# Kernel optimization log

Hardware: AMD Instinct MI355X
Metric: run time of the kernel (lower is better)

The kernel has to match this reference:

```python
import jax, jax.numpy as jnp
import numpy as np

HIDDEN = 4096
NH = 32          # num attention heads
NKV = 8          # num key/value heads
HD = HIDDEN // NH  # 128
THETA = 10000.0
WINDOW = 4096    # sliding window hard-coded in forward


def _rotate_half(x):
    x1, x2 = jnp.split(x, 2, axis=-1)
    return jnp.concatenate((-x2, x1), axis=-1)


def setup_inputs() -> dict:
    key = jax.random.key(0)
    ks = jax.random.split(key, 5)
    B, S = 1, 2048
    hidden_states = jax.random.normal(ks[0], (B, S, HIDDEN), jnp.float32)
    position_ids = jnp.broadcast_to(jnp.arange(S, dtype=jnp.int64), (B, S))
    s = 0.02
    q_w = jax.random.normal(ks[1], (HIDDEN, NH * HD), jnp.float32) * s
    k_w = jax.random.normal(ks[2], (HIDDEN, NKV * HD), jnp.float32) * s
    v_w = jax.random.normal(ks[3], (HIDDEN, NKV * HD), jnp.float32) * s
    o_w = jax.random.normal(ks[4], (NH * HD, HIDDEN), jnp.float32) * s
    return {"hidden_states": hidden_states, "position_ids": position_ids,
            "q_w": q_w, "k_w": k_w, "v_w": v_w, "o_w": o_w}


def reference(hidden_states, position_ids, q_w, k_w, v_w, o_w):
    B, S, _ = hidden_states.shape
    # projections (bias=False), split heads -> [B, H, S, D]
    q = (hidden_states @ q_w).reshape(B, S, NH, HD).transpose(0, 2, 1, 3)
    k = (hidden_states @ k_w).reshape(B, S, NKV, HD).transpose(0, 2, 1, 3)
    v = (hidden_states @ v_w).reshape(B, S, NKV, HD).transpose(0, 2, 1, 3)

    # rotary embedding cache (MistralRotaryEmbedding)
    inv_freq = 1.0 / (THETA ** (jnp.arange(0, HD, 2, dtype=jnp.float32) / HD))
    t = jnp.arange(S, dtype=jnp.float32)
    freqs = t[:, None] * inv_freq[None, :]           # [S, HD/2]
    emb = jnp.concatenate((freqs, freqs), axis=-1)   # [S, HD]
    cos = jnp.cos(emb)[position_ids][:, None]        # [B, 1, S, HD]
    sin = jnp.sin(emb)[position_ids][:, None]
    q = q * cos + _rotate_half(q) * sin
    k = k * cos + _rotate_half(k) * sin

    # GQA repeat_kv: [B, NKV, S, D] -> [B, NH, S, D]
    rep = NH // NKV
    k = jnp.repeat(k, rep, axis=1)
    v = jnp.repeat(v, rep, axis=1)

    # scores + sliding-window causal mask
    scale = 1.0 / np.sqrt(HD).astype(np.float32)
    w = jnp.einsum("bhqd,bhkd->bhqk", q, k) * scale  # [B, NH, S, S]
    i = jnp.arange(S)[:, None]
    j = jnp.arange(S)[None, :]
    allowed = (j <= i) & ((i - j) < WINDOW)
    neg = jnp.finfo(jnp.float32).min
    w = w + jnp.where(allowed, 0.0, neg)[None, None]

    # fp32 softmax (upcast as in HF Mistral)
    w = jax.nn.softmax(w.astype(jnp.float32), axis=-1).astype(q.dtype)

    out = jnp.einsum("bhqk,bhkd->bhqd", w, v)        # [B, NH, S, D]
    out = out.transpose(0, 2, 1, 3).reshape(B, S, NH * HD)
    return out @ o_w                                  # [B, S, HIDDEN]
```

## Files before the change

kernel.cpp:

```cpp
#include <hip/hip_runtime.h>
#include <hip/hip_bf16.h>

#define S 2048
#define HID 4096
#define NH 32
#define NKV 8
#define HD 128
#define QKVN 6144

typedef __attribute__((ext_vector_type(8))) short bf16x8;
typedef __attribute__((ext_vector_type(4))) float f32x4;
typedef __attribute__((ext_vector_type(8))) unsigned short u16x8;
typedef __attribute__((ext_vector_type(4))) unsigned short u16x4;

#define GLOAD16(src, dst)                                                        \
  __builtin_amdgcn_global_load_lds(                                              \
      (const __attribute__((address_space(1))) unsigned int*)(src),              \
      (__attribute__((address_space(3))) unsigned int*)(dst), 16, 0, 0)

__device__ __forceinline__ unsigned short f2bf(float f) {
  union { float f; unsigned u; } c; c.f = f;
  unsigned u = c.u;
  return (unsigned short)((u + 0x7FFFu + ((u >> 16) & 1u)) >> 16);
}
__device__ __forceinline__ float bf2f(unsigned short h) {
  union { unsigned u; float f; } c; c.u = ((unsigned)h) << 16;
  return c.f;
}

__global__ void convert_kernel(const float* __restrict__ in,
                               unsigned short* __restrict__ out, int n4) {
  int i = blockIdx.x * blockDim.x + threadIdx.x;
  if (i < n4) {
    float4 v = ((const float4*)in)[i];
    ushort4 o;
    o.x = f2bf(v.x); o.y = f2bf(v.y); o.z = f2bf(v.z); o.w = f2bf(v.w);
    ((ushort4*)out)[i] = o;
  }
}

__global__ void transpose_convert(const float* __restrict__ in,
                                  unsigned short* __restrict__ out, int N) {
  __shared__ float tile[32][33];
  int tx = threadIdx.x, ty = threadIdx.y;
  int n0 = blockIdx.x * 32, k0 = blockIdx.y * 32;
#pragma unroll
  for (int i = 0; i < 32; i += 8)
    tile[ty + i][tx] = in[(size_t)(k0 + ty + i) * N + n0 + tx];
  __syncthreads();
#pragma unroll
  for (int i = 0; i < 32; i += 8)
    out[(size_t)(n0 + ty + i) * HID + k0 + tx] = f2bf(tile[tx][ty + i]);
}

__device__ __forceinline__ void storeC(unsigned short* C, size_t idx, float v) { C[idx] = f2bf(v); }
__device__ __forceinline__ void storeC(float* C, size_t idx, float v) { C[idx] = v; }

template <typename OutT>
__launch_bounds__(256, 2)
__global__ void gemm_bt(const unsigned short* __restrict__ A,
                        const unsigned short* __restrict__ Bt,
                        OutT* __restrict__ C, int K, int ldc) {
  __shared__ unsigned short As[2][2][128 * 32];
  __shared__ unsigned short Bs[2][2][128 * 32];
  const int tid = threadIdx.x, lane = tid & 63, w = tid >> 6;
  const int wr = w >> 1, wc = w & 1;
  const int m0 = blockIdx.y * 128, n0 = blockIdx.x * 128;
  const int lq = lane & 15, g = lane >> 4;
  const int swz8 = (g ^ (lq & 3) ^ ((lq >> 2) & 3)) << 3;

  f32x4 acc[4][4] = {};
  const int NT = K >> 6;

  auto STAGE_PAIR = [&](int bb, int ss, int kt) {
#pragma unroll
    for (int i = 0; i < 2; ++i) {
      int ci = tid + i * 256;
      int row = ci >> 2;
      int jl = (((ci & 3) ^ (row & 3) ^ ((row >> 2) & 3))) << 3;
      GLOAD16(A + (size_t)(m0 + row) * K + kt + ss * 32 + jl, &As[bb][ss][ci * 8]);
      GLOAD16(Bt + (size_t)(n0 + row) * K + kt + ss * 32 + jl, &Bs[bb][ss][ci * 8]);
    }
  };

  STAGE_PAIR(0, 0, 0);
  STAGE_PAIR(0, 1, 0);

  for (int t = 0; t < NT; ++t) {
    const int c = t & 1;
    const bool more = (t + 1) < NT;
    const int kt1 = (t + 1) << 6;
#pragma unroll
    for (int s = 0; s < 2; ++s) {
      if (s == 0 || more) asm volatile("s_waitcnt vmcnt(4)" ::: "memory");
      else                asm volatile("s_waitcnt vmcnt(0)" ::: "memory");
      __builtin_amdgcn_s_barrier();

      bf16x8 af[4], bfr[4];
#pragma unroll
      for (int mi = 0; mi < 4; ++mi)
        af[mi] = *(const bf16x8*)&As[c][s][(wr * 64 + mi * 16 + lq) * 32 + swz8];
#pragma unroll
      for (int ni = 0; ni < 4; ++ni)
        bfr[ni] = *(const bf16x8*)&Bs[c][s][(wc * 64 + ni * 16 + lq) * 32 + swz8];

      if (more) STAGE_PAIR(c ^ 1, s, kt1);

      asm volatile("s_waitcnt lgkmcnt(0)" ::: "memory");
      __builtin_amdgcn_sched_barrier(0);
      __builtin_amdgcn_s_setprio(1);
#pragma unroll
      for (int mi = 0; mi < 4; ++mi)
#pragma unroll
        for (int ni = 0; ni < 4; ++ni)
          acc[mi][ni] = __builtin_amdgcn_mfma_f32_16x16x32_bf16(af[mi], bfr[ni], acc[mi][ni], 0, 0, 0);
      __builtin_amdgcn_s_setprio(0);
    }
  }

#pragma unroll
  for (int mi = 0; mi < 4; ++mi) {
#pragma unroll
    for (int ni = 0; ni < 4; ++ni) {
      int row = m0 + wr * 64 + mi * 16 + g * 4;
      int col = n0 + wc * 64 + ni * 16 + lq;
#pragma unroll
      for (int r = 0; r < 4; ++r)
        storeC(C, (size_t)(row + r) * ldc + col, acc[mi][ni][r]);
    }
  }
}

__global__ void rope_kernel(unsigned short* __restrict__ qkv) {
  int idx = blockIdx.x * blockDim.x + threadIdx.x;
  int d = idx & 63;
  int h = (idx >> 6) % (NH + NKV);
  int s = (idx >> 6) / (NH + NKV);
  size_t base = (size_t)s * QKVN + (h < NH ? h * HD : NH * HD + (h - NH) * HD);
  float invf = __expf(-(float)d * (1.0f / 64.0f) * 9.210340371976184f);
  float ang = (float)s * invf;
  float c, sn;
  __sincosf(ang, &sn, &c);
  float x1 = bf2f(qkv[base + d]);
  float x2 = bf2f(qkv[base + d + 64]);
  float o1 = x1 * c - x2 * sn;
  float o2 = x2 * c + x1 * sn;
  if (h < NH) {
    o1 *= 0.08838834764831845f;
    o2 *= 0.08838834764831845f;
  }
  qkv[base + d] = f2bf(o1);
  qkv[base + d + 64] = f2bf(o2);
}

__launch_bounds__(512, 4)
__global__ void attn_kernel(const unsigned short* __restrict__ qkv,
                            unsigned short* __restrict__ ao) {
  __shared__ unsigned short Ks[2][64 * 128];
  __shared__ unsigned short Vt[128 * 88];
  __shared__ unsigned short Ps[8][16 * 88];

  const int tid = threadIdx.x, lane = tid & 63, w = tid >> 6;
  const int b = blockIdx.x;
  const int h = blockIdx.y;
  const int qblk = (h < 16) ? (15 - b) : b;
  const int kh = h >> 2;
  const int lq = lane & 15, g = lane >> 4;
  const int qbase = qblk * 128 + w * 16;
  const size_t koff = (size_t)NH * HD + (size_t)kh * HD;
  const size_t voff = (size_t)(NH + NKV) * HD + (size_t)kh * HD;

  bf16x8 qf[4];
  {
    const unsigned short* qp = qkv + (size_t)(qbase + lq) * QKVN + (size_t)h * HD + g * 8;
#pragma unroll
    for (int ks = 0; ks < 4; ++ks) qf[ks] = *(const bf16x8*)(qp + ks * 32);
  }

  f32x4 o[8] = {};
  float m = -1e30f;
  float l = 0.f;

  auto KSTAGE = [&](int bb, int kv0) {
#pragma unroll
    for (int i = 0; i < 2; ++i) {
      int kvk = (w * 2 + i) * 4 + (lane >> 4);
      int chl = (lane & 15) ^ (kvk & 7);
      GLOAD16(qkv + (size_t)(kv0 + kvk) * QKVN + koff + chl * 8, &Ks[bb][(w * 2 + i) * 512]);
    }
  };
  const int vd0 = (tid & 31) * 4;
  const int vkv = (tid >> 5) * 4;
  u16x4 vr[4];
  auto VLOAD = [&](int kv0) {
#pragma unroll
    for (int i = 0; i < 4; ++i)
      vr[i] = *(const u16x4*)(qkv + (size_t)(kv0 + vkv + i) * QKVN + voff + vd0);
  };
  auto VWRITE = [&]() {
#pragma unroll
    for (int j = 0; j < 4; ++j) {
      const int d = vd0 + j;
      const int vswz = ((d >> 3) & 3) << 1;
      const int vcol = (((vkv >> 2) ^ vswz) << 2);
      u16x4 val = {vr[0][j], vr[1][j], vr[2][j], vr[3][j]};
      *(u16x4*)&Vt[d * 88 + vcol] = val;
    }
  };

  unsigned short* Pw = &Ps[w][0];
  const int nt = qblk * 2 + 2;

  KSTAGE(0, 0);
  VLOAD(0);
  int cur = 0;
  for (int t = 0; t < nt; ++t) {
    const int kv0 = t * 64;
    __syncthreads();
    VWRITE();
    __syncthreads();
    if (t + 1 < nt) { KSTAGE(cur ^ 1, kv0 + 64); VLOAD(kv0 + 64); }

    const int nraw = qbase + 16 - kv0;
    const int nact = nraw > 64 ? 64 : nraw;

    f32x4 sc[4];
    __builtin_amdgcn_s_setprio(1);
#pragma unroll
    for (int st = 0; st < 4; ++st) {
      if (st * 16 < nact) {
        f32x4 s = {};
#pragma unroll
        for (int ks = 0; ks < 4; ++ks) {
          const bf16x8 kf = *(const bf16x8*)
              &Ks[cur][(st * 16 + lq) * 128 + (((ks * 4 + g) ^ (lq & 7)) << 3)];
          s = __builtin_amdgcn_mfma_f32_16x16x32_bf16(kf, qf[ks], s, 0, 0, 0);
        }
        sc[st] = s;
      } else {
        sc[st] = (f32x4){-1e30f, -1e30f, -1e30f, -1e30f};
      }
    }
    __builtin_amdgcn_s_setprio(0);
    if (nraw < 79) {
      const int q = qbase + lq;
#pragma unroll
      for (int st = 0; st < 4; ++st) {
        int kv = kv0 + st * 16 + g * 4;
#pragma unroll
        for (int r = 0; r < 4; ++r)
          if (kv + r > q) sc[st][r] = -1e30f;
      }
    }

    float mn = fmaxf(fmaxf(fmaxf(sc[0][0], sc[0][1]), fmaxf(sc[0][2], sc[0][3])),
                     fmaxf(fmaxf(sc[1][0], sc[1][1]), fmaxf(sc[1][2], sc[1][3])));
    mn = fmaxf(mn, fmaxf(fmaxf(fmaxf(sc[2][0], sc[2][1]), fmaxf(sc[2][2], sc[2][3])),
                         fmaxf(fmaxf(sc[3][0], sc[3][1]), fmaxf(sc[3][2], sc[3][3]))));
    mn = fmaxf(mn, __shfl_xor(mn, 16, 64));
    mn = fmaxf(mn, __shfl_xor(mn, 32, 64));
    const bool need = __any(mn > m);
    const float m2 = fmaxf(m, mn);
    const float alpha = __expf(m - m2);
    m = m2;
    float rs = 0.f;
#pragma unroll
    for (int st = 0; st < 4; ++st)
#pragma unroll
      for (int r = 0; r < 4; ++r) {
        float p = __expf(sc[st][r] - m2);
        sc[st][r] = p;
        rs += p;
      }
    rs += __shfl_xor(rs, 16, 64);
    rs += __shfl_xor(rs, 32, 64);
    l = l * alpha + rs;

    if (need) {
      float alphaR[4];
#pragma unroll
      for (int r = 0; r < 4; ++r) alphaR[r] = __shfl(alpha, g * 4 + r, 64);
#pragma unroll
      for (int p = 0; p < 8; ++p)
#pragma unroll
        for (int r = 0; r < 4; ++r) o[p][r] *= alphaR[r];
    }

#pragma unroll
    for (int st = 0; st < 4; ++st) {
      u16x4 val = {f2bf(sc[st][0]), f2bf(sc[st][1]), f2bf(sc[st][2]), f2bf(sc[st][3])};
      *(u16x4*)&Pw[lq * 88 + st * 16 + g * 4] = val;
    }

    const int nks = nact > 0 ? (nact + 31) >> 5 : 0;
    __builtin_amdgcn_s_setprio(1);
    for (int ks = 0; ks < nks; ++ks) {
      const bf16x8 pf = *(const bf16x8*)&Pw[lq * 88 + ks * 32 + g * 8];
#pragma unroll
      for (int p = 0; p < 8; ++p) {
        const int d = p * 16 + lq;
        const int rswz = ((d >> 3) & 3) << 1;
        const int kvc = (ks * 8 + g * 2) ^ rswz;
        const bf16x8 vf = *(const bf16x8*)&Vt[d * 88 + (kvc << 2)];
        o[p] = __builtin_amdgcn_mfma_f32_16x16x32_bf16(pf, vf, o[p], 0, 0, 0);
      }
    }
    __builtin_amdgcn_s_setprio(0);

    cur ^= 1;
  }

  float invR[4];
#pragma unroll
  for (int r = 0; r < 4; ++r) invR[r] = 1.0f / __shfl(l, g * 4 + r, 64);
#pragma unroll
  for (int p = 0; p < 8; ++p)
#pragma unroll
    for (int r = 0; r < 4; ++r)
      ao[(size_t)(qbase + g * 4 + r) * (NH * HD) + (size_t)h * HD + p * 16 + lq] =
          f2bf(o[p][r] * invR[r]);
}

extern "C" void kernel_launch(void* const* d_in, const int* in_sizes, int n_in,
                              void* d_out, int out_size, void* d_ws, size_t ws_size,
                              hipStream_t stream) {
  const float* X  = (const float*)d_in[0];
  const float* qw = (const float*)d_in[2];
  const float* kw = (const float*)d_in[3];
  const float* vw = (const float*)d_in[4];
  const float* ow = (const float*)d_in[5];
  float* out = (float*)d_out;

  char* ws = (char*)d_ws;
  unsigned short* Xb  = (unsigned short*)(ws);
  unsigned short* Wt  = (unsigned short*)(ws + (size_t)(16u << 20));
  unsigned short* QKV = (unsigned short*)(ws + (size_t)(64u << 20));
  unsigned short* AO  = (unsigned short*)(ws + (size_t)(88u << 20));
  unsigned short* OWt = (unsigned short*)(ws);

  dim3 tb(32, 8);

  convert_kernel<<<(S * HID / 4 + 255) / 256, 256, 0, stream>>>(X, Xb, S * HID / 4);
  transpose_convert<<<dim3(HID / 32, HID / 32), tb, 0, stream>>>(qw, Wt, HID);
  transpose_convert<<<dim3((NKV * HD) / 32, HID / 32), tb, 0, stream>>>(kw, Wt + (size_t)(NH * HD) * HID, NKV * HD);
  transpose_convert<<<dim3((NKV * HD) / 32, HID / 32), tb, 0, stream>>>(vw, Wt + (size_t)(NH + NKV) * HD * HID, NKV * HD);
  gemm_bt<unsigned short><<<dim3(QKVN / 128, S / 128), 256, 0, stream>>>(Xb, Wt, QKV, HID, QKVN);
  transpose_convert<<<dim3(HID / 32, HID / 32), tb, 0, stream>>>(ow, OWt, HID);
  rope_kernel<<<(S * (NH + NKV) * 64) / 256, 256, 0, stream>>>(QKV);
  attn_kernel<<<dim3(16, NH), 512, 0, stream>>>(QKV, AO);
  gemm_bt<float><<<dim3(HID / 128, S / 128), 256, 0, stream>>>(AO, OWt, out, HID, HID);
}
```

Before: 361.3 us.

## Use 256x256-tile 8-wave GEMM with quarter-staged double buffering for QKV projection

Adds a new GEMM kernel with 256x256 output tiles, 512 threads and 8 waves, each wave computing a 128x64 sub-tile. It double-buffers LDS and interleaves four half-tile global-to-LDS stages with four MFMA quadrants, separated by barriers and explicit waitcnts. It is used only for the QKV projection, to raise arithmetic intensity and overlap loads with compute. The trade-off is fewer blocks (24x8=192 on a 256-CU part), so occupancy and tail utilisation may suffer, and the larger tile uses 128KB of LDS.

```diff
diff --git a/kernel.cpp b/kernel.cpp
--- a/kernel.cpp
+++ b/kernel.cpp
@@ -129,6 +129,109 @@
         storeC(C, (size_t)(row + r) * ldc + col, acc[mi][ni][r]);
     }
   }
+}
+
+template <typename OutT>
+__launch_bounds__(512, 1)
+__global__ void gemm256q(const unsigned short* __restrict__ A,
+                         const unsigned short* __restrict__ Bt,
+                         OutT* __restrict__ C, int K, int ldc) {
+  __shared__ unsigned short As[2][2][128 * 64];
+  __shared__ unsigned short Bs[2][2][128 * 64];
+  const int tid = threadIdx.x, lane = tid & 63, w = tid >> 6;
+  const int wm = w >> 2, wn = w & 3;
+  const int m0 = blockIdx.y * 256, n0 = blockIdx.x * 256;
+  const int lq = lane & 15, g = lane >> 4;
+  const int sw = lq & 7;
+
+  f32x4 acc[8][4] = {};
+  bf16x8 af[4][2], bfr[4][2];
+  const int NT = K >> 6;
+
+  auto STAGE_HALF = [&](const unsigned short* src, int row_base, unsigned short* lds, int kt) {
+#pragma unroll
+    for (int i = 0; i < 2; ++i) {
+      int ci = tid + i * 512;
+      int r = ci >> 3, j = ci & 7;
+      int jl = j ^ (r & 7);
+      GLOAD16(src + (size_t)(row_base + r) * K + kt + jl * 8, lds + ci * 8);
+    }
+  };
+
+#define READ_A(QM)                                                               \
+  _Pragma("unroll") for (int mi2 = 0; mi2 < 4; ++mi2)                            \
+  _Pragma("unroll") for (int ks = 0; ks < 2; ++ks)                               \
+    af[mi2][ks] = *(const bf16x8*)&Aw[((QM) * 64 + mi2 * 16 + lq) * 64 +         \
+                                      (((ks * 4 + g) ^ sw) << 3)];
+
+#define READ_B2(NI0)                                                             \
+  _Pragma("unroll") for (int ni2 = 0; ni2 < 2; ++ni2)                            \
+  _Pragma("unroll") for (int ks = 0; ks < 2; ++ks)                               \
+    bfr[(NI0) + ni2][ks] = *(const bf16x8*)&Bw[(rb0 + ((NI0) + ni2) * 16 + lq) * 64 + \
+                                               (((ks * 4 + g) ^ sw) << 3)];
+
+#define MFMA_Q(QM, QN)                                                           \
+  __builtin_amdgcn_s_setprio(1);                                                 \
+  _Pragma("unroll") for (int mi2 = 0; mi2 < 4; ++mi2)                            \
+  _Pragma("unroll") for (int ni2 = 0; ni2 < 2; ++ni2)                            \
+  _Pragma("unroll") for (int ks = 0; ks < 2; ++ks)                               \
+    acc[(QM) * 4 + mi2][(QN) * 2 + ni2] = __builtin_amdgcn_mfma_f32_16x16x32_bf16( \
+        af[mi2][ks], bfr[(QN) * 2 + ni2][ks],                                    \
+        acc[(QM) * 4 + mi2][(QN) * 2 + ni2], 0, 0, 0);                           \
+  __builtin_amdgcn_s_setprio(0);
+
+  STAGE_HALF(A, m0, &As[0][0][0], 0);
+  STAGE_HALF(A, m0 + 128, &As[0][1][0], 0);
+  STAGE_HALF(Bt, n0, &Bs[0][0][0], 0);
+  STAGE_HALF(Bt, n0 + 128, &Bs[0][1][0], 0);
+
+  for (int t = 0; t < NT; ++t) {
+    const int c = t & 1;
+    const bool more = (t + 1) < NT;
+    const int kt1 = (t + 1) << 6;
+    const unsigned short* Aw = &As[c][wm][0];
+    const unsigned short* Bw = &Bs[c][wn >> 1][0];
+    const int rb0 = (wn & 1) * 64;
+
+    if ((w & 2) == 0) asm volatile("s_waitcnt vmcnt(2)" ::: "memory");
+    else              asm volatile("s_waitcnt vmcnt(0)" ::: "memory");
+    __builtin_amdgcn_s_barrier();
+    if (more) STAGE_HALF(A, m0, &As[c ^ 1][0][0], kt1);
+    READ_A(0); READ_B2(0);
+    asm volatile("s_waitcnt lgkmcnt(0)" ::: "memory");
+    __builtin_amdgcn_sched_barrier(0);
+    MFMA_Q(0, 0);
+    __builtin_amdgcn_s_barrier();
+    if (more) STAGE_HALF(A, m0 + 128, &As[c ^ 1][1][0], kt1);
+    READ_B2(2);
+    asm volatile("s_waitcnt lgkmcnt(0)" ::: "memory");
+    __builtin_amdgcn_sched_barrier(0);
+    MFMA_Q(0, 1);
+    __builtin_amdgcn_s_barrier();
+    if (more) STAGE_HALF(Bt, n0, &Bs[c ^ 1][0][0], kt1);
+    READ_A(1);
+    asm volatile("s_waitcnt lgkmcnt(0)" ::: "memory");
+    __builtin_amdgcn_sched_barrier(0);
+    MFMA_Q(1, 0);
+    __builtin_amdgcn_s_barrier();
+    if (more) STAGE_HALF(Bt, n0 + 128, &Bs[c ^ 1][1][0], kt1);
+    MFMA_Q(1, 1);
+  }
+
+#undef READ_A
+#undef READ_B2
+#undef MFMA_Q
+
+#pragma unroll
+  for (int mi = 0; mi < 8; ++mi)
+#pragma unroll
+    for (int ni = 0; ni < 4; ++ni) {
+      int row = m0 + wm * 128 + mi * 16 + g * 4;
+      int col = n0 + wn * 64 + ni * 16 + lq;
+#pragma unroll
+      for (int r = 0; r < 4; ++r)
+        storeC(C, (size_t)(row + r) * ldc + col, acc[mi][ni][r]);
+    }
 }
 
 __global__ void rope_kernel(unsigned short* __restrict__ qkv) {
@@ -344,7 +447,7 @@
   transpose_convert<<<dim3(HID / 32, HID / 32), tb, 0, stream>>>(qw, Wt, HID);
   transpose_convert<<<dim3((NKV * HD) / 32, HID / 32), tb, 0, stream>>>(kw, Wt + (size_t)(NH * HD) * HID, NKV * HD);
   transpose_convert<<<dim3((NKV * HD) / 32, HID / 32), tb, 0, stream>>>(vw, Wt + (size_t)(NH + NKV) * HD * HID, NKV * HD);
-  gemm_bt<unsigned short><<<dim3(QKVN / 128, S / 128), 256, 0, stream>>>(Xb, Wt, QKV, HID, QKVN);
+  gemm256q<unsigned short><<<dim3(QKVN / 256, S / 256), 512, 0, stream>>>(Xb, Wt, QKV, HID, QKVN);
   transpose_convert<<<dim3(HID / 32, HID / 32), tb, 0, stream>>>(ow, OWt, HID);
   rope_kernel<<<(S * (NH + NKV) * 64) / 256, 256, 0, stream>>>(QKV);
   attn_kernel<<<dim3(16, NH), 512, 0, stream>>>(QKV, AO);
```

New measurement: 384.2 us. +6.3%, slower.
